# Optimization experiments

Hardware: AMD Instinct MI355X
Metric: run time of the kernel (lower is better)

## Reference

```python
import jax, jax.numpy as jnp
import numpy as np
import math

B, P, N, DM, H, DK, DH, DF = 2, 12, 170, 64, 8, 8, 32, 256
SQ = math.sqrt(DK)

def _ln(x, g, b):
    m = jnp.mean(x, -1, keepdims=True)
    v = jnp.var(x, -1, keepdims=True)
    return (x - m) / jnp.sqrt(v + 1e-5) * g + b

def _nozero_softmax(s):
    # faithful to nozero_softmax: mask = (s != 0), max over full row, +1e-5 in denom
    mask = (s != 0).astype(s.dtype)
    e = jnp.exp(s - jnp.max(s, -1, keepdims=True)) * mask
    return e / (jnp.sum(e, -1, keepdims=True) + 1e-5)

def _meta(c, w1, b1, w2, b2):
    # MetaLearner: [B,P,N,DM] -> [3,B,P,N,H,DK,DM]
    h = jax.nn.relu(c @ w1 + b1) @ w2 + b2
    h = h.reshape(c.shape[:3] + (3, H, DK, DM))
    return jnp.moveaxis(h, 3, 0)

def _mhlin(W, x):
    # multihead_linear_transform: per-position meta weight applied to x
    return jnp.einsum('bpnhkd,bpnd->bpnhk', W, x)

def _gdc(data, W1, W2):
    # Gated_Dynamic_Connection (noGC=False). data: [G,B,P,N,C]
    d = jnp.moveaxis(data, 0, 3)  # [B,P,N,G,C]
    a = jnp.einsum('bpngc,gcd->bpngd', d, W1)
    s = jax.nn.softmax(jax.nn.relu(jnp.einsum('bpngc,gcd->bpngd', d, W2)), axis=3)
    return jnp.sum(a * s, axis=3)  # [B,P,N,DM]

def _swish_gate(x, out, wg, bg, wo, bo):
    h = (x @ wg + bg) * out
    return (h * jax.nn.sigmoid(h)) @ wo + bo

def _spatial(Q, K, V, T):
    # adjacency-masked spatial attention. Dense-masked form is exactly the
    # scatter-into-zeros buffer of the original: zero where T==0, QK/sqrt(dk) on edges.
    s = jnp.einsum('bpihk,bpjhk->bphij', Q, K) / SQ
    Tb = T if T.ndim == 2 else T[:, :, None]  # adaptive graph [B,P,1,N,N]
    s = s * (Tb != 0)
    alpha = _nozero_softmax(s) * Tb
    return jnp.einsum('bphij,bpjhk->hbpik', alpha, V)  # [H,B,P,N,DK]

def _temporal(Q, K, V):
    s = jnp.einsum('bqnhk,bpnhk->bnhqp', Q, K) / SQ
    alpha = jax.nn.softmax(s, -1)
    return jnp.einsum('bnhqp,bpnhk->hbqnk', alpha, V)  # [H,B,P,N,DK]

def _retnet(Q, K, V, D):
    # multihead_temporal_regnet with g=1 leading dim folded in
    r = jnp.einsum('bqnhk,bpnhk->bnhqp', Q, K) / SQ
    r = r * D  # D: [H,P,P] causal decay
    rs = jnp.maximum(jnp.abs(jnp.sum(r, -1, keepdims=True)), 1.0)
    r = r / rs
    return jnp.einsum('bnhqp,bpnhk->hbqnk', r, V)  # [H,B,P,N,DK]

def _forward(x, c_x, enc, T, A, D, mr_w1, mr_b1, mr_w2, mr_b2, ms0_w1, ms0_b1, ms0_w2, ms0_b2, ms1_w1, ms1_b1, ms1_w2, ms1_b2, gr_W1, gr_W2, gs0_W1, gs0_W2, gs1_W1, gs1_W2, g2_W1, g2_W2, ge_W1, ge_W2, swr_wg, swr_bg, swr_wo, swr_bo, sws_wg, sws_bg, sws_wo, sws_bo, swe_wg, swe_bg, swe_wo, swe_bo, lnr_g, lnr_b, lns_g, lns_b, lne_g, lne_b, lnf_g, lnf_b, wq, wk, wv, f_w1, f_b1, f_w2, f_b2):
    # 1) RetNet-style temporal self retention (meta-learned QKV)
    W = _meta(c_x, mr_w1, mr_b1, mr_w2, mr_b2)
    o = _gdc(_retnet(_mhlin(W[0], x), _mhlin(W[1], x), _mhlin(W[2], x), D), gr_W1, gr_W2)
    o = _swish_gate(x, o, swr_wg, swr_bg, swr_wo, swr_bo)
    x1 = _ln(o + x, lnr_g, lnr_b)
    # 2) Spatial self attention: predefined graph + adaptive graph branches
    W0 = _meta(c_x, ms0_w1, ms0_b1, ms0_w2, ms0_b2)
    o0 = _gdc(_spatial(_mhlin(W0[0], x1), _mhlin(W0[1], x1), _mhlin(W0[2], x1), T), gs0_W1, gs0_W2)
    W1m = _meta(c_x, ms1_w1, ms1_b1, ms1_w2, ms1_b2)
    o1 = _gdc(_spatial(_mhlin(W1m[0], x1), _mhlin(W1m[1], x1), _mhlin(W1m[2], x1), A), gs1_W1, gs1_W2)
    o = _gdc(jnp.stack([o0, o1], 0), g2_W1, g2_W2)
    o = _swish_gate(x1, o, sws_wg, sws_bg, sws_wo, sws_bo)
    x2 = _ln(o + x1, lns_g, lns_b)
    # 3) Temporal encoder-decoder attention
    q = (x2 @ wq).reshape(B, P, N, H, DK)
    k = (enc @ wk).reshape(B, P, N, H, DK)
    v = (enc @ wv).reshape(B, P, N, H, DK)
    o = _gdc(_temporal(q, k, v), ge_W1, ge_W2)
    o = _swish_gate(x2, o, swe_wg, swe_bg, swe_wo, swe_bo)
    x3 = _ln(o + x2, lne_g, lne_b)
    # 4) FFN
    o = jax.nn.relu(x3 @ f_w1 + f_b1) @ f_w2 + f_b2
    return _ln(o + x3, lnf_g, lnf_b)


def setup_inputs() -> dict:
    key = jax.random.key(0)
    ks = iter(jax.random.split(key, 100))
    def rn(shape, s=0.05):
        return (jax.random.normal(next(ks), shape) * s).astype(jnp.float32)
    inp = {}
    inp['x'] = jax.random.normal(next(ks), (B, P, N, DM), jnp.float32)
    inp['c_x'] = jax.random.normal(next(ks), (B, P, N, DM), jnp.float32)
    inp['enc'] = jax.random.normal(next(ks), (B, P, N, DM), jnp.float32)
    mT = jax.random.uniform(next(ks), (N, N)) < 0.1
    inp['T'] = (jax.random.uniform(next(ks), (N, N)) * mT).astype(jnp.float32)
    mA = jax.random.uniform(next(ks), (B, P, N, N)) < 0.05
    inp['A'] = (jax.random.uniform(next(ks), (B, P, N, N)) * mA).astype(jnp.float32)
    q = np.arange(P)
    gam = 1.0 - 2.0 ** (-5.0 - np.arange(H))
    Dm = np.where(q[:, None] >= q[None, :], gam[:, None, None] ** (q[:, None] - q[None, :]), 0.0)
    inp['D'] = jnp.asarray(Dm, jnp.float32)  # [H,P,P]
    for p in ['mr', 'ms0', 'ms1']:
        inp[p + '_w1'] = rn((DM, DH)); inp[p + '_b1'] = jnp.zeros((DH,), jnp.float32)
        inp[p + '_w2'] = rn((DH, 3 * H * DK * DM)); inp[p + '_b2'] = jnp.zeros((3 * H * DK * DM,), jnp.float32)
    for p in ['gr', 'gs0', 'gs1', 'ge']:
        inp[p + '_W1'] = rn((H, DK, DM)); inp[p + '_W2'] = rn((H, DK, DM))
    inp['g2_W1'] = rn((2, DM, DM)); inp['g2_W2'] = rn((2, DM, DM))
    for p in ['swr', 'sws', 'swe']:
        inp[p + '_wg'] = rn((DM, DM)); inp[p + '_bg'] = jnp.zeros((DM,), jnp.float32)
        inp[p + '_wo'] = rn((DM, DM)); inp[p + '_bo'] = jnp.zeros((DM,), jnp.float32)
    for p in ['lnr', 'lns', 'lne', 'lnf']:
        inp[p + '_g'] = jnp.ones((DM,), jnp.float32); inp[p + '_b'] = jnp.zeros((DM,), jnp.float32)
    inp['wq'] = rn((DM, DM)); inp['wk'] = rn((DM, DM)); inp['wv'] = rn((DM, DM))
    inp['f_w1'] = rn((DM, DF)); inp['f_b1'] = jnp.zeros((DF,), jnp.float32)
    inp['f_w2'] = rn((DF, DM)); inp['f_b2'] = jnp.zeros((DM,), jnp.float32)
    return inp


def reference(x, c_x, enc, T, A, D, mr_w1, mr_b1, mr_w2, mr_b2, ms0_w1, ms0_b1, ms0_w2, ms0_b2, ms1_w1, ms1_b1, ms1_w2, ms1_b2, gr_W1, gr_W2, gs0_W1, gs0_W2, gs1_W1, gs1_W2, g2_W1, g2_W2, ge_W1, ge_W2, swr_wg, swr_bg, swr_wo, swr_bo, sws_wg, sws_bg, sws_wo, sws_bo, swe_wg, swe_bg, swe_wo, swe_bo, lnr_g, lnr_b, lns_g, lns_b, lne_g, lne_b, lnf_g, lnf_b, wq, wk, wv, f_w1, f_b1, f_w2, f_b2):
    return _forward(x, c_x, enc, T, A, D, mr_w1, mr_b1, mr_w2, mr_b2, ms0_w1, ms0_b1, ms0_w2, ms0_b2, ms1_w1, ms1_b1, ms1_w2, ms1_b2, gr_W1, gr_W2, gs0_W1, gs0_W2, gs1_W1, gs1_W2, g2_W1, g2_W2, ge_W1, ge_W2, swr_wg, swr_bg, swr_wo, swr_bo, sws_wg, sws_bg, sws_wo, sws_bo, swe_wg, swe_bg, swe_wo, swe_bo, lnr_g, lnr_b, lns_g, lns_b, lne_g, lne_b, lnf_g, lnf_b, wq, wk, wv, f_w1, f_b1, f_w2, f_b2)
```

## Files before the change

### kernel.cpp

```cpp
#include <hip/hip_runtime.h>
#include <hip/hip_bf16.h>
#include <math.h>

namespace {

constexpr int B_ = 2, P_ = 12, N_ = 170, DM_ = 64, H_ = 8, DK_ = 8, DH_ = 32, DF_ = 256;
constexpr int T_ = B_ * P_ * N_;
constexpr float SQRT_DK = 2.8284271247461903f;

constexpr int NG_ = 12;
constexpr int NC_ = 66;
constexpr int WFRAG_G = NG_ * NC_ * 64 * 8;

typedef __attribute__((ext_vector_type(4))) short short4v;
typedef __attribute__((ext_vector_type(8))) short short8v;
typedef __attribute__((ext_vector_type(4))) float float4v;

__device__ __forceinline__ unsigned short f2bf(float x) {
    union { float f; unsigned int u; } c; c.f = x;
    unsigned int r = (c.u + 0x7FFFu + ((c.u >> 16) & 1u)) >> 16;
    return (unsigned short)r;
}

__global__ void k_hr3(const float* __restrict__ c_x,
                      const float* __restrict__ w1a, const float* __restrict__ b1a,
                      const float* __restrict__ w1b, const float* __restrict__ b1b,
                      const float* __restrict__ w1c, const float* __restrict__ b1c,
                      float* __restrict__ hra, float* __restrict__ hrb,
                      float* __restrict__ hrc) {
    int z = blockIdx.y;
    const float* w1 = z == 0 ? w1a : (z == 1 ? w1b : w1c);
    const float* b1 = z == 0 ? b1a : (z == 1 ? b1b : b1c);
    float* hr = z == 0 ? hra : (z == 1 ? hrb : hrc);
    int idx = blockIdx.x * 256 + threadIdx.x;
    if (idx >= T_ * DH_) return;
    int t = idx / DH_, j = idx % DH_;
    float acc = b1[j];
    const float* cx = c_x + t * DM_;
    #pragma unroll
    for (int d = 0; d < DM_; ++d) acc += cx[d] * w1[d * DH_ + j];
    hr[idx] = fmaxf(acc, 0.f);
}

__global__ void k_wconv(const float* __restrict__ w2a, const float* __restrict__ b2a,
                        const float* __restrict__ w2b, const float* __restrict__ b2b,
                        const float* __restrict__ w2c, const float* __restrict__ b2c,
                        unsigned short* __restrict__ Wfrag) {
    int idx = blockIdx.x * 256 + threadIdx.x;
    if (idx >= 3 * NG_ * NC_ * 64) return;
    int lane = idx & 63;
    int c = (idx >> 6) % NC_;
    int ng = (idx >> 6) / NC_ % NG_;
    int g = idx / (64 * NC_ * NG_);
    const float* w2 = g == 0 ? w2a : (g == 1 ? w2b : w2c);
    const float* b2 = g == 0 ? b2a : (g == 1 ? b2b : b2c);
    int m = ng * 16 + (lane & 15);
    int u = c >> 1;
    int d0 = (c & 1) * 32 + (lane >> 4) * 8;
    const float* src = (u < DH_) ? (w2 + u * 12288 + m * 64 + d0) : (b2 + m * 64 + d0);
    short8v o;
    #pragma unroll
    for (int j = 0; j < 8; ++j) o[j] = (short)f2bf(src[j]);
    *(short8v*)(Wfrag + (size_t)idx * 8) = o;
}

__global__ __launch_bounds__(256) void k_meta_gemm2(
    const float* __restrict__ hr0, const float* __restrict__ hr1,
    const float* __restrict__ xin,
    const unsigned short* __restrict__ Wf0, const unsigned short* __restrict__ Wf1,
    float* __restrict__ out0, float* __restrict__ out1) {
    const int bz = blockIdx.z;
    const float* hr = bz ? hr1 : hr0;
    const unsigned short* Wf = bz ? Wf1 : Wf0;
    float* out = bz ? out1 : out0;

    const int tid = threadIdx.x;
    const int wv = tid >> 6, lane = tid & 63;
    const int l15 = lane & 15, quad = lane >> 4;
    const int g16 = blockIdx.x * 4 + wv;
    if (g16 >= 255) return;
    const int t = g16 * 16 + l15;
    const int nb = blockIdx.y;

    const float* xp = xin + t * 64 + quad * 8;
    float4v xa = *(const float4v*)(xp);
    float4v xb = *(const float4v*)(xp + 4);
    float4v xc = *(const float4v*)(xp + 32);
    float4v xd = *(const float4v*)(xp + 36);
    float xr[16] = {xa.x, xa.y, xa.z, xa.w, xb.x, xb.y, xb.z, xb.w,
                    xc.x, xc.y, xc.z, xc.w, xd.x, xd.y, xd.z, xd.w};

    const float* hrp = hr + t * 32;
    float4v acc[4] = {{0.f,0.f,0.f,0.f},{0.f,0.f,0.f,0.f},
                      {0.f,0.f,0.f,0.f},{0.f,0.f,0.f,0.f}};

    const unsigned short* wb = Wf + ((size_t)(nb * 4) * NC_ * 64 + lane) * 8;
    const size_t qstride = (size_t)NC_ * 64 * 8;
    const size_t cstride = 64 * 8;

    for (int u = 0; u < 33; ++u) {
        float hrv = (u < DH_) ? hrp[u] : 1.0f;
        short8v a0, a1;
        #pragma unroll
        for (int j = 0; j < 8; ++j) {
            a0[j] = (short)f2bf(hrv * xr[j]);
            a1[j] = (short)f2bf(hrv * xr[8 + j]);
        }
        const unsigned short* wc = wb + (size_t)(2 * u) * cstride;
        #pragma unroll
        for (int q = 0; q < 4; ++q) {
            short8v b0 = *(const short8v*)(wc + q * qstride);
            short8v b1 = *(const short8v*)(wc + q * qstride + cstride);
            acc[q] = __builtin_amdgcn_mfma_f32_16x16x32_bf16(a0, b0, acc[q], 0, 0, 0);
            acc[q] = __builtin_amdgcn_mfma_f32_16x16x32_bf16(a1, b1, acc[q], 0, 0, 0);
        }
    }

    #pragma unroll
    for (int q = 0; q < 4; ++q) {
        #pragma unroll
        for (int r = 0; r < 4; ++r) {
            int tt = g16 * 16 + quad * 4 + r;
            out[tt * 192 + nb * 64 + q * 16 + l15] = acc[q][r];
        }
    }
}

__global__ __launch_bounds__(256) void k_retnet(const float* __restrict__ qkv,
                                                const float* __restrict__ Dm,
                                                float* __restrict__ att) {
    const int bn = blockIdx.x;
    const int b = bn / N_, n = bn % N_;
    __shared__ float S[12][192];
    __shared__ float Ds[8 * 145];
    const int tid = threadIdx.x;
    for (int e = tid; e < 12 * 192; e += 256) {
        int p = e / 192, c = e % 192;
        S[p][c] = qkv[((size_t)((b * P_ + p) * N_ + n)) * 192 + c];
    }
    for (int e = tid; e < 1152; e += 256) {
        Ds[(e / 144) * 145 + (e % 144)] = Dm[e];
    }
    __syncthreads();
    const int qq = tid >> 6;
    const int lane = tid & 63;
    const int h = lane >> 3, k = lane & 7;
    for (int q = qq; q < P_; q += 4) {
        float Qv = S[q][h * 8 + k];
        float r[P_];
        float rsum = 0.f;
        #pragma unroll
        for (int p = 0; p < P_; ++p) {
            float prod = Qv * S[p][64 + h * 8 + k];
            prod += __shfl_xor(prod, 1, 64);
            prod += __shfl_xor(prod, 2, 64);
            prod += __shfl_xor(prod, 4, 64);
            float s = (prod / SQRT_DK) * Ds[h * 145 + q * 12 + p];
            r[p] = s; rsum += s;
        }
        float rs = fmaxf(fabsf(rsum), 1.0f);
        float acc = 0.f;
        #pragma unroll
        for (int p = 0; p < P_; ++p) acc += (r[p] / rs) * S[p][128 + h * 8 + k];
        att[((size_t)((b * P_ + q) * N_ + n)) * 64 + lane] = acc;
    }
}

__global__ __launch_bounds__(256) void k_temporal(const float* __restrict__ qkv,
                                                  float* __restrict__ att) {
    const int bn = blockIdx.x;
    const int b = bn / N_, n = bn % N_;
    __shared__ float S[12][192];
    const int tid = threadIdx.x;
    for (int e = tid; e < 12 * 192; e += 256) {
        int p = e / 192, c = e % 192;
        S[p][c] = qkv[((size_t)((b * P_ + p) * N_ + n)) * 192 + c];
    }
    __syncthreads();
    const int qq = tid >> 6;
    const int lane = tid & 63;
    const int h = lane >> 3, k = lane & 7;
    for (int q = qq; q < P_; q += 4) {
        float Qv = S[q][h * 8 + k];
        float s[P_];
        float mx = -1e30f;
        #pragma unroll
        for (int p = 0; p < P_; ++p) {
            float prod = Qv * S[p][64 + h * 8 + k];
            prod += __shfl_xor(prod, 1, 64);
            prod += __shfl_xor(prod, 2, 64);
            prod += __shfl_xor(prod, 4, 64);
            float v = prod / SQRT_DK;
            s[p] = v; mx = fmaxf(mx, v);
        }
        float den = 0.f, acc = 0.f;
        #pragma unroll
        for (int p = 0; p < P_; ++p) {
            float e = expf(s[p] - mx);
            den += e;
            acc += e * S[p][128 + h * 8 + k];
        }
        att[((size_t)((b * P_ + q) * N_ + n)) * 64 + lane] = acc / den;
    }
}

__global__ __launch_bounds__(256) void k_spatial4(
    const float* __restrict__ qkvA, const float* __restrict__ qkvB,
    const float* __restrict__ Tm, const float* __restrict__ Am,
    float* __restrict__ attA, float* __restrict__ attB) {
    const int bp = blockIdx.x;
    const int h = blockIdx.y;
    const int g = blockIdx.z >> 2;
    const int ic = blockIdx.z & 3;
    const float* qkv = g ? qkvB : qkvA;
    float* att = g ? attB : attA;

    __shared__ float sKt[8][192];
    __shared__ float sV[192][8];
    __shared__ float sW[4][192];

    const int tid = threadIdx.x;
    for (int e = tid; e < 384; e += 256) {
        int j = e >> 1, kh = (e & 1) * 4;
        float4v k4 = {0.f, 0.f, 0.f, 0.f}, v4 = k4;
        if (j < N_) {
            const float* row = qkv + (size_t)(bp * N_ + j) * 192 + h * 8 + kh;
            k4 = *(const float4v*)(row + 64);
            v4 = *(const float4v*)(row + 128);
        }
        sKt[kh + 0][j] = k4.x;
        sKt[kh + 1][j] = k4.y;
        sKt[kh + 2][j] = k4.z;
        sKt[kh + 3][j] = k4.w;
        *(float4v*)&sV[j][kh] = v4;
    }
    __syncthreads();

    const int wv = tid >> 6;
    const int lane = tid & 63;
    const int j8 = lane >> 3, kk = lane & 7;

    const int i0 = ic * 43;
    const int i1 = (i0 + 43 < N_) ? (i0 + 43) : N_;

    for (int i = i0 + wv; i < i1; i += 4) {
        const float* qrow = qkv + (size_t)(bp * N_ + i) * 192 + h * 8;
        float4v qa = *(const float4v*)qrow;
        float4v qb = *(const float4v*)(qrow + 4);
        float Qi[8] = {qa.x, qa.y, qa.z, qa.w, qb.x, qb.y, qb.z, qb.w};
        const float* Trow = g ? (Am + (size_t)(bp * N_ + i) * N_) : (Tm + (size_t)i * N_);

        float sloc[3], tloc[3];
        float mx = -1e30f;
        #pragma unroll
        for (int c = 0; c < 3; ++c) {
            int j = c * 64 + lane;
            float tv = 0.f, s = -1e30f;
            if (j < N_) {
                tv = Trow[j];
                if (tv != 0.f) {
                    float dot = 0.f;
                    #pragma unroll
                    for (int k = 0; k < 8; ++k) dot += Qi[k] * sKt[k][j];
                    s = dot / SQRT_DK;
                } else {
                    s = 0.f;
                }
            }
            sloc[c] = s; tloc[c] = tv;
            mx = fmaxf(mx, s);
        }
        #pragma unroll
        for (int off = 1; off < 64; off <<= 1) mx = fmaxf(mx, __shfl_xor(mx, off, 64));

        float den = 0.f;
        #pragma unroll
        for (int c = 0; c < 3; ++c) {
            float s = sloc[c];
            float e = (s != 0.f) ? expf(s - mx) : 0.f;
            den += e;
            sW[wv][c * 64 + lane] = e * tloc[c];
        }
        #pragma unroll
        for (int off = 1; off < 64; off <<= 1) den += __shfl_xor(den, off, 64);

        float acc = 0.f;
        #pragma unroll 4
        for (int j = j8; j < 192; j += 8) acc += sW[wv][j] * sV[j][kk];
        acc += __shfl_xor(acc, 8, 64);
        acc += __shfl_xor(acc, 16, 64);
        acc += __shfl_xor(acc, 32, 64);
        if (lane < 8)
            att[(size_t)(bp * N_ + i) * 64 + h * 8 + lane] = acc / (den + 1e-5f);
    }
}

__device__ __forceinline__ float gdc8(const float* dv, const float* W1,
                                      const float* W2, int dm) {
    float a[8], s[8];
    #pragma unroll
    for (int g = 0; g < 8; ++g) {
        float aa = 0.f, ss = 0.f;
        #pragma unroll
        for (int c = 0; c < 8; ++c) {
            float d = dv[g * 8 + c];
            aa += d * W1[(g * 8 + c) * 64 + dm];
            ss += d * W2[(g * 8 + c) * 64 + dm];
        }
        a[g] = aa; s[g] = fmaxf(ss, 0.f);
    }
    float mx = s[0];
    #pragma unroll
    for (int g = 1; g < 8; ++g) mx = fmaxf(mx, s[g]);
    float den = 0.f, o = 0.f;
    #pragma unroll
    for (int g = 0; g < 8; ++g) { float e = expf(s[g] - mx); den += e; o += a[g] * e; }
    return o / den;
}

__device__ __forceinline__ float ln_out(float r, int dm, const float* g, const float* b) {
    float m = r, m2 = r * r;
    #pragma unroll
    for (int off = 32; off; off >>= 1) { m += __shfl_xor(m, off, 64); m2 += __shfl_xor(m2, off, 64); }
    m *= (1.f / 64.f); m2 *= (1.f / 64.f);
    float var = m2 - m * m;
    return (r - m) * rsqrtf(var + 1e-5f) * g[dm] + b[dm];
}

__global__ __launch_bounds__(64) void k_gsl(const float* __restrict__ att, const float* __restrict__ xin,
    const float* W1, const float* W2,
    const float* wg, const float* bg,
    const float* wo, const float* bo,
    const float* lng, const float* lnb, float* __restrict__ xout) {
    int t = blockIdx.x, dm = threadIdx.x;
    __shared__ float dv[64], xv[64], swv[64];
    dv[dm] = att[t * 64 + dm];
    xv[dm] = xin[t * 64 + dm];
    __syncthreads();
    float o = gdc8(dv, W1, W2, dm);
    float hg = bg[dm];
    #pragma unroll
    for (int d = 0; d < 64; ++d) hg += xv[d] * wg[d * 64 + dm];
    hg *= o;
    swv[dm] = hg / (1.f + expf(-hg));
    __syncthreads();
    float ov = bo[dm];
    #pragma unroll
    for (int d = 0; d < 64; ++d) ov += swv[d] * wo[d * 64 + dm];
    float r = ov + xv[dm];
    xout[t * 64 + dm] = ln_out(r, dm, lng, lnb);
}

__global__ __launch_bounds__(64) void k_spatial_fuse(
    const float* __restrict__ att0, const float* __restrict__ att1, const float* __restrict__ x1,
    const float* gs0_W1, const float* gs0_W2,
    const float* gs1_W1, const float* gs1_W2,
    const float* g2_W1, const float* g2_W2,
    const float* wg, const float* bg,
    const float* wo, const float* bo,
    const float* lng, const float* lnb, float* __restrict__ xout) {
    int t = blockIdx.x, dm = threadIdx.x;
    __shared__ float d0[64], d1[64], o0s[64], o1s[64], xv[64], swv[64];
    d0[dm] = att0[t * 64 + dm];
    d1[dm] = att1[t * 64 + dm];
    xv[dm] = x1[t * 64 + dm];
    __syncthreads();
    o0s[dm] = gdc8(d0, gs0_W1, gs0_W2, dm);
    o1s[dm] = gdc8(d1, gs1_W1, gs1_W2, dm);
    __syncthreads();
    float a0 = 0.f, s0 = 0.f, a1 = 0.f, s1 = 0.f;
    #pragma unroll
    for (int c = 0; c < 64; ++c) {
        a0 += o0s[c] * g2_W1[c * 64 + dm];
        s0 += o0s[c] * g2_W2[c * 64 + dm];
        a1 += o1s[c] * g2_W1[(64 + c) * 64 + dm];
        s1 += o1s[c] * g2_W2[(64 + c) * 64 + dm];
    }
    s0 = fmaxf(s0, 0.f); s1 = fmaxf(s1, 0.f);
    float mx = fmaxf(s0, s1);
    float e0 = expf(s0 - mx), e1 = expf(s1 - mx);
    float o = (a0 * e0 + a1 * e1) / (e0 + e1);
    float hg = bg[dm];
    #pragma unroll
    for (int d = 0; d < 64; ++d) hg += xv[d] * wg[d * 64 + dm];
    hg *= o;
    swv[dm] = hg / (1.f + expf(-hg));
    __syncthreads();
    float ov = bo[dm];
    #pragma unroll
    for (int d = 0; d < 64; ++d) ov += swv[d] * wo[d * 64 + dm];
    float r = ov + xv[dm];
    xout[t * 64 + dm] = ln_out(r, dm, lng, lnb);
}

__global__ __launch_bounds__(64) void k_qkvproj(const float* __restrict__ x2,
    const float* __restrict__ enc,
    const float* wq, const float* wk, const float* wv,
    float* __restrict__ qkv) {
    int t = blockIdx.x, dm = threadIdx.x;
    __shared__ float xv[64], ev[64];
    xv[dm] = x2[t * 64 + dm];
    ev[dm] = enc[t * 64 + dm];
    __syncthreads();
    float aq = 0.f, ak = 0.f, av = 0.f;
    #pragma unroll
    for (int d = 0; d < 64; ++d) {
        aq += xv[d] * wq[d * 64 + dm];
        ak += ev[d] * wk[d * 64 + dm];
        av += ev[d] * wv[d * 64 + dm];
    }
    qkv[t * 192 + dm] = aq;
    qkv[t * 192 + 64 + dm] = ak;
    qkv[t * 192 + 128 + dm] = av;
}

__global__ __launch_bounds__(64) void k_ffn(const float* __restrict__ x3,
    const float* w1, const float* b1,
    const float* w2, const float* b2,
    const float* lng, const float* lnb,
    float* __restrict__ out) {
    int t = blockIdx.x, dm = threadIdx.x;
    __shared__ float xv[64], hv[256];
    xv[dm] = x3[t * 64 + dm];
    __syncthreads();
    #pragma unroll
    for (int e = 0; e < 4; ++e) {
        int j = e * 64 + dm;
        float a = b1[j];
        #pragma unroll
        for (int d = 0; d < 64; ++d) a += xv[d] * w1[d * 256 + j];
        hv[j] = fmaxf(a, 0.f);
    }
    __syncthreads();
    float a = b2[dm];
    for (int j = 0; j < 256; ++j) a += hv[j] * w2[j * 64 + dm];
    float r = a + xv[dm];
    out[t * 64 + dm] = ln_out(r, dm, lng, lnb);
}

}

extern "C" void kernel_launch(void* const* d_in, const int* in_sizes, int n_in,
                              void* d_out, int out_size, void* d_ws, size_t ws_size,
                              hipStream_t stream) {
    (void)in_sizes; (void)n_in; (void)out_size; (void)ws_size;
    const float* x    = (const float*)d_in[0];
    const float* c_x  = (const float*)d_in[1];
    const float* enc  = (const float*)d_in[2];
    const float* Tm   = (const float*)d_in[3];
    const float* Am   = (const float*)d_in[4];
    const float* Dm   = (const float*)d_in[5];
    const float* mr_w1 = (const float*)d_in[6];
    const float* mr_b1 = (const float*)d_in[7];
    const float* mr_w2 = (const float*)d_in[8];
    const float* mr_b2 = (const float*)d_in[9];
    const float* ms0_w1 = (const float*)d_in[10];
    const float* ms0_b1 = (const float*)d_in[11];
    const float* ms0_w2 = (const float*)d_in[12];
    const float* ms0_b2 = (const float*)d_in[13];
    const float* ms1_w1 = (const float*)d_in[14];
    const float* ms1_b1 = (const float*)d_in[15];
    const float* ms1_w2 = (const float*)d_in[16];
    const float* ms1_b2 = (const float*)d_in[17];
    const float* gr_W1 = (const float*)d_in[18];
    const float* gr_W2 = (const float*)d_in[19];
    const float* gs0_W1 = (const float*)d_in[20];
    const float* gs0_W2 = (const float*)d_in[21];
    const float* gs1_W1 = (const float*)d_in[22];
    const float* gs1_W2 = (const float*)d_in[23];
    const float* g2_W1 = (const float*)d_in[24];
    const float* g2_W2 = (const float*)d_in[25];
    const float* ge_W1 = (const float*)d_in[26];
    const float* ge_W2 = (const float*)d_in[27];
    const float* swr_wg = (const float*)d_in[28];
    const float* swr_bg = (const float*)d_in[29];
    const float* swr_wo = (const float*)d_in[30];
    const float* swr_bo = (const float*)d_in[31];
    const float* sws_wg = (const float*)d_in[32];
    const float* sws_bg = (const float*)d_in[33];
    const float* sws_wo = (const float*)d_in[34];
    const float* sws_bo = (const float*)d_in[35];
    const float* swe_wg = (const float*)d_in[36];
    const float* swe_bg = (const float*)d_in[37];
    const float* swe_wo = (const float*)d_in[38];
    const float* swe_bo = (const float*)d_in[39];
    const float* lnr_g = (const float*)d_in[40];
    const float* lnr_b = (const float*)d_in[41];
    const float* lns_g = (const float*)d_in[42];
    const float* lns_b = (const float*)d_in[43];
    const float* lne_g = (const float*)d_in[44];
    const float* lne_b = (const float*)d_in[45];
    const float* lnf_g = (const float*)d_in[46];
    const float* lnf_b = (const float*)d_in[47];
    const float* wq = (const float*)d_in[48];
    const float* wk = (const float*)d_in[49];
    const float* wv = (const float*)d_in[50];
    const float* f_w1 = (const float*)d_in[51];
    const float* f_b1 = (const float*)d_in[52];
    const float* f_w2 = (const float*)d_in[53];
    const float* f_b2 = (const float*)d_in[54];

    float* ws   = (float*)d_ws;
    float* hr   = ws;
    float* hr2  = hr   + T_ * DH_;
    float* qkva = hr2  + T_ * DH_;
    float* qkvb = qkva + T_ * 192;
    float* atta = qkvb + T_ * 192;
    float* attb = atta + T_ * DM_;
    float* x1f  = attb + T_ * DM_;
    float* x2f  = x1f  + T_ * DM_;
    float* x3f  = x2f  + T_ * DM_;
    unsigned short* Wfrag = (unsigned short*)(x3f + T_ * DM_);
    float* hr_r = attb;

    k_wconv<<<(3 * NG_ * NC_ * 64 + 255) / 256, 256, 0, stream>>>(
        mr_w2, mr_b2, ms0_w2, ms0_b2, ms1_w2, ms1_b2, Wfrag);

    k_hr3<<<dim3(510, 3), 256, 0, stream>>>(c_x, mr_w1, mr_b1, ms0_w1, ms0_b1,
                                            ms1_w1, ms1_b1, hr_r, hr, hr2);

    k_meta_gemm2<<<dim3(64, 3, 1), 256, 0, stream>>>(
        hr_r, hr_r, x, Wfrag, Wfrag, qkva, qkva);
    k_retnet<<<B_ * N_, 256, 0, stream>>>(qkva, Dm, atta);
    k_gsl<<<T_, 64, 0, stream>>>(atta, x, gr_W1, gr_W2, swr_wg, swr_bg, swr_wo, swr_bo,
                                 lnr_g, lnr_b, x1f);

    k_meta_gemm2<<<dim3(64, 3, 2), 256, 0, stream>>>(
        hr, hr2, x1f, Wfrag + WFRAG_G, Wfrag + 2 * WFRAG_G, qkva, qkvb);
    k_spatial4<<<dim3(B_ * P_, H_, 8), 256, 0, stream>>>(qkva, qkvb, Tm, Am, atta, attb);
    k_spatial_fuse<<<T_, 64, 0, stream>>>(atta, attb, x1f, gs0_W1, gs0_W2, gs1_W1, gs1_W2,
                                          g2_W1, g2_W2, sws_wg, sws_bg, sws_wo, sws_bo,
                                          lns_g, lns_b, x2f);

    k_qkvproj<<<T_, 64, 0, stream>>>(x2f, enc, wq, wk, wv, qkva);
    k_temporal<<<B_ * N_, 256, 0, stream>>>(qkva, atta);
    k_gsl<<<T_, 64, 0, stream>>>(atta, x2f, ge_W1, ge_W2, swe_wg, swe_bg, swe_wo, swe_bo,
                                 lne_g, lne_b, x3f);

    k_ffn<<<T_, 64, 0, stream>>>(x3f, f_w1, f_b1, f_w2, f_b2, lnf_g, lnf_b, (float*)d_out);
}
```

Measured before the change: 344.7 us.

## Port token-wise dense layers to bf16 MFMA with pre-packed weight fragments

Replaces the five per-token scalar kernels (gated dynamic connection, swish-gate, spatial fuse, QKV projection, FFN with layer norm) with MFMA 16x16x32 bf16 kernels that process 16 tokens per wave. A new conversion kernel packs all small weight matrices into bf16 fragment layout, with block-diagonal padding for the grouped GDC weights, so they feed MFMA directly. The aim is to cut scalar FMA work and the 4080 tiny-block launches. In exchange, activations and weights are rounded to bf16, which lowers precision. The GDC softmax also drops max-subtraction, relying on small logits.

After: 345.0 us. Within noise of the previous version (+0.1%).

```diff
diff --git a/kernel.cpp b/kernel.cpp
--- a/kernel.cpp
+++ b/kernel.cpp
@@ -11,6 +11,8 @@
 constexpr int NG_ = 12;
 constexpr int NC_ = 66;
 constexpr int WFRAG_G = NG_ * NC_ * 64 * 8;
+
+constexpr int WSM_UNITS = 53;
 
 typedef __attribute__((ext_vector_type(4))) short short4v;
 typedef __attribute__((ext_vector_type(8))) short short8v;
@@ -20,6 +22,18 @@
     union { float f; unsigned int u; } c; c.f = x;
     unsigned int r = (c.u + 0x7FFFu + ((c.u >> 16) & 1u)) >> 16;
     return (unsigned short)r;
+}
+
+__device__ __forceinline__ short8v afrag(const float* rowbase, int kc, int quad) {
+    const float* p = rowbase + kc * 32 + quad * 8;
+    float4v a = *(const float4v*)p;
+    float4v b = *(const float4v*)(p + 4);
+    short8v f;
+    f[0] = (short)f2bf(a.x); f[1] = (short)f2bf(a.y);
+    f[2] = (short)f2bf(a.z); f[3] = (short)f2bf(a.w);
+    f[4] = (short)f2bf(b.x); f[5] = (short)f2bf(b.y);
+    f[6] = (short)f2bf(b.z); f[7] = (short)f2bf(b.w);
+    return f;
 }
 
 __global__ void k_hr3(const float* __restrict__ c_x,
@@ -64,6 +78,69 @@
     *(short8v*)(Wfrag + (size_t)idx * 8) = o;
 }
 
+__global__ void k_wconv2(
+    const float* swr_wg, const float* swr_wo, const float* sws_wg, const float* sws_wo,
+    const float* swe_wg, const float* swe_wo,
+    const float* wq, const float* wk, const float* wv,
+    const float* f_w1, const float* f_w2,
+    const float* g2_W1, const float* g2_W2,
+    const float* gr_W1, const float* gr_W2, const float* gs0_W1, const float* gs0_W2,
+    const float* gs1_W1, const float* gs1_W2, const float* ge_W1, const float* ge_W2,
+    unsigned short* __restrict__ Wsm) {
+    const int job = blockIdx.y;
+    const int idx = blockIdx.x * 256 + threadIdx.x;
+    const float* s1 = nullptr; const float* s2 = nullptr;
+    int dst = 0, KC = 2, NG = 4, N = 64, kind = 0;
+    switch (job) {
+        case 0:  s1 = swr_wg; dst = 0; break;
+        case 1:  s1 = swr_wo; dst = 1; break;
+        case 2:  s1 = sws_wg; dst = 2; break;
+        case 3:  s1 = sws_wo; dst = 3; break;
+        case 4:  s1 = swe_wg; dst = 4; break;
+        case 5:  s1 = swe_wo; dst = 5; break;
+        case 6:  s1 = wq; dst = 6; break;
+        case 7:  s1 = wk; dst = 7; break;
+        case 8:  s1 = wv; dst = 8; break;
+        case 9:  s1 = f_w1; dst = 9;  NG = 16; N = 256; break;
+        case 10: s1 = f_w2; dst = 13; KC = 8; break;
+        case 11: s1 = g2_W1;        dst = 17; break;
+        case 12: s1 = g2_W1 + 4096; dst = 18; break;
+        case 13: s1 = g2_W2;        dst = 19; break;
+        case 14: s1 = g2_W2 + 4096; dst = 20; break;
+        case 15: s1 = gr_W1;  s2 = gr_W2;  dst = 21; kind = 1; break;
+        case 16: s1 = gs0_W1; s2 = gs0_W2; dst = 29; kind = 1; break;
+        case 17: s1 = gs1_W1; s2 = gs1_W2; dst = 37; kind = 1; break;
+        default: s1 = ge_W1;  s2 = ge_W2;  dst = 45; kind = 1; break;
+    }
+    if (kind == 0) {
+        if (idx >= NG * KC * 64) return;
+        int lane = idx & 63;
+        int kc = (idx >> 6) % KC, ng = (idx >> 6) / KC;
+        int krow = kc * 32 + (lane >> 4) * 8;
+        int n = ng * 16 + (lane & 15);
+        short8v o;
+        #pragma unroll
+        for (int j = 0; j < 8; ++j) o[j] = (short)f2bf(s1[(krow + j) * N + n]);
+        *(short8v*)(Wsm + (size_t)dst * 4096 + (size_t)idx * 8) = o;
+    } else {
+        if (idx >= 8 * 4 * 64) return;
+        int lane = idx & 63;
+        int ng = (idx >> 6) & 3, g = idx >> 8;
+        int quad = lane >> 4, n = ng * 16 + (lane & 15);
+        short8v o1 = {0,0,0,0,0,0,0,0}, o2 = {0,0,0,0,0,0,0,0};
+        if (quad == (g & 3)) {
+            #pragma unroll
+            for (int j = 0; j < 8; ++j) {
+                o1[j] = (short)f2bf(s1[(g * 8 + j) * 64 + n]);
+                o2[j] = (short)f2bf(s2[(g * 8 + j) * 64 + n]);
+            }
+        }
+        size_t off = (size_t)dst * 4096 + (size_t)idx * 8;
+        *(short8v*)(Wsm + off) = o1;
+        *(short8v*)(Wsm + off + 16384) = o2;
+    }
+}
+
 __global__ __launch_bounds__(256) void k_meta_gemm2(
     const float* __restrict__ hr0, const float* __restrict__ hr1,
     const float* __restrict__ xin,
@@ -295,147 +372,387 @@
     }
 }
 
-__device__ __forceinline__ float gdc8(const float* dv, const float* W1,
-                                      const float* W2, int dm) {
-    float a[8], s[8];
-    #pragma unroll
+__device__ __forceinline__ void gdc_mfma(const short8v* attf,
+                                         const unsigned short* gdcW, int lane,
+                                         float4v* num, float4v* den) {
+    #pragma unroll
+    for (int q = 0; q < 4; ++q) {
+        num[q] = (float4v){0.f, 0.f, 0.f, 0.f};
+        den[q] = (float4v){0.f, 0.f, 0.f, 0.f};
+    }
     for (int g = 0; g < 8; ++g) {
-        float aa = 0.f, ss = 0.f;
-        #pragma unroll
-        for (int c = 0; c < 8; ++c) {
-            float d = dv[g * 8 + c];
-            aa += d * W1[(g * 8 + c) * 64 + dm];
-            ss += d * W2[(g * 8 + c) * 64 + dm];
-        }
-        a[g] = aa; s[g] = fmaxf(ss, 0.f);
-    }
-    float mx = s[0];
-    #pragma unroll
-    for (int g = 1; g < 8; ++g) mx = fmaxf(mx, s[g]);
-    float den = 0.f, o = 0.f;
-    #pragma unroll
-    for (int g = 0; g < 8; ++g) { float e = expf(s[g] - mx); den += e; o += a[g] * e; }
-    return o / den;
-}
-
-__device__ __forceinline__ float ln_out(float r, int dm, const float* g, const float* b) {
-    float m = r, m2 = r * r;
-    #pragma unroll
-    for (int off = 32; off; off >>= 1) { m += __shfl_xor(m, off, 64); m2 += __shfl_xor(m2, off, 64); }
-    m *= (1.f / 64.f); m2 *= (1.f / 64.f);
-    float var = m2 - m * m;
-    return (r - m) * rsqrtf(var + 1e-5f) * g[dm] + b[dm];
-}
-
-__global__ __launch_bounds__(64) void k_gsl(const float* __restrict__ att, const float* __restrict__ xin,
-    const float* W1, const float* W2,
-    const float* wg, const float* bg,
-    const float* wo, const float* bo,
-    const float* lng, const float* lnb, float* __restrict__ xout) {
-    int t = blockIdx.x, dm = threadIdx.x;
-    __shared__ float dv[64], xv[64], swv[64];
-    dv[dm] = att[t * 64 + dm];
-    xv[dm] = xin[t * 64 + dm];
-    __syncthreads();
-    float o = gdc8(dv, W1, W2, dm);
-    float hg = bg[dm];
-    #pragma unroll
-    for (int d = 0; d < 64; ++d) hg += xv[d] * wg[d * 64 + dm];
-    hg *= o;
-    swv[dm] = hg / (1.f + expf(-hg));
-    __syncthreads();
-    float ov = bo[dm];
-    #pragma unroll
-    for (int d = 0; d < 64; ++d) ov += swv[d] * wo[d * 64 + dm];
-    float r = ov + xv[dm];
-    xout[t * 64 + dm] = ln_out(r, dm, lng, lnb);
-}
-
-__global__ __launch_bounds__(64) void k_spatial_fuse(
-    const float* __restrict__ att0, const float* __restrict__ att1, const float* __restrict__ x1,
-    const float* gs0_W1, const float* gs0_W2,
-    const float* gs1_W1, const float* gs1_W2,
-    const float* g2_W1, const float* g2_W2,
-    const float* wg, const float* bg,
-    const float* wo, const float* bo,
-    const float* lng, const float* lnb, float* __restrict__ xout) {
-    int t = blockIdx.x, dm = threadIdx.x;
-    __shared__ float d0[64], d1[64], o0s[64], o1s[64], xv[64], swv[64];
-    d0[dm] = att0[t * 64 + dm];
-    d1[dm] = att1[t * 64 + dm];
-    xv[dm] = x1[t * 64 + dm];
-    __syncthreads();
-    o0s[dm] = gdc8(d0, gs0_W1, gs0_W2, dm);
-    o1s[dm] = gdc8(d1, gs1_W1, gs1_W2, dm);
-    __syncthreads();
-    float a0 = 0.f, s0 = 0.f, a1 = 0.f, s1 = 0.f;
-    #pragma unroll
-    for (int c = 0; c < 64; ++c) {
-        a0 += o0s[c] * g2_W1[c * 64 + dm];
-        s0 += o0s[c] * g2_W2[c * 64 + dm];
-        a1 += o1s[c] * g2_W1[(64 + c) * 64 + dm];
-        s1 += o1s[c] * g2_W2[(64 + c) * 64 + dm];
-    }
-    s0 = fmaxf(s0, 0.f); s1 = fmaxf(s1, 0.f);
-    float mx = fmaxf(s0, s1);
-    float e0 = expf(s0 - mx), e1 = expf(s1 - mx);
-    float o = (a0 * e0 + a1 * e1) / (e0 + e1);
-    float hg = bg[dm];
-    #pragma unroll
-    for (int d = 0; d < 64; ++d) hg += xv[d] * wg[d * 64 + dm];
-    hg *= o;
-    swv[dm] = hg / (1.f + expf(-hg));
-    __syncthreads();
-    float ov = bo[dm];
-    #pragma unroll
-    for (int d = 0; d < 64; ++d) ov += swv[d] * wo[d * 64 + dm];
-    float r = ov + xv[dm];
-    xout[t * 64 + dm] = ln_out(r, dm, lng, lnb);
-}
-
-__global__ __launch_bounds__(64) void k_qkvproj(const float* __restrict__ x2,
-    const float* __restrict__ enc,
-    const float* wq, const float* wk, const float* wv,
+        const unsigned short* wb = gdcW + ((size_t)(g * 4) * 64 + lane) * 8;
+        short8v af = attf[g >> 2];
+        float4v a[4], s[4];
+        #pragma unroll
+        for (int q = 0; q < 4; ++q) {
+            a[q] = (float4v){0.f, 0.f, 0.f, 0.f};
+            s[q] = (float4v){0.f, 0.f, 0.f, 0.f};
+        }
+        #pragma unroll
+        for (int q = 0; q < 4; ++q) {
+            short8v b1 = *(const short8v*)(wb + q * 512);
+            short8v b2 = *(const short8v*)(wb + 16384 + q * 512);
+            a[q] = __builtin_amdgcn_mfma_f32_16x16x32_bf16(af, b1, a[q], 0, 0, 0);
+            s[q] = __builtin_amdgcn_mfma_f32_16x16x32_bf16(af, b2, s[q], 0, 0, 0);
+        }
+        #pragma unroll
+        for (int q = 0; q < 4; ++q) {
+            #pragma unroll
+            for (int r = 0; r < 4; ++r) {
+                float e = __expf(fmaxf(s[q][r], 0.f));
+                den[q][r] += e;
+                num[q][r] += a[q][r] * e;
+            }
+        }
+    }
+}
+
+__global__ __launch_bounds__(256) void k_gsl5(
+    const float* __restrict__ att, const float* __restrict__ xin,
+    const unsigned short* __restrict__ gdcW,
+    const unsigned short* __restrict__ gateW, const unsigned short* __restrict__ woW,
+    const float* __restrict__ bg, const float* __restrict__ bo,
+    const float* __restrict__ lng, const float* __restrict__ lnb,
+    float* __restrict__ xout) {
+    __shared__ unsigned short swl[4][16][72];
+    const int tid = threadIdx.x, wv = tid >> 6, lane = tid & 63;
+    const int l15 = lane & 15, quad = lane >> 4;
+    const int g16 = blockIdx.x * 4 + wv;
+    if (g16 >= 255) return;
+    const int t = g16 * 16 + l15;
+
+    short8v attf[2], xf[2];
+    #pragma unroll
+    for (int kc = 0; kc < 2; ++kc) {
+        attf[kc] = afrag(att + (size_t)t * 64, kc, quad);
+        xf[kc]   = afrag(xin + (size_t)t * 64, kc, quad);
+    }
+
+    float4v num[4], den[4];
+    gdc_mfma(attf, gdcW, lane, num, den);
+
+    float4v hg[4];
+    #pragma unroll
+    for (int q = 0; q < 4; ++q) hg[q] = (float4v){0.f, 0.f, 0.f, 0.f};
+    #pragma unroll
+    for (int kc = 0; kc < 2; ++kc)
+        #pragma unroll
+        for (int q = 0; q < 4; ++q)
+            hg[q] = __builtin_amdgcn_mfma_f32_16x16x32_bf16(
+                xf[kc], *(const short8v*)(gateW + ((size_t)(q * 2 + kc) * 64 + lane) * 8),
+                hg[q], 0, 0, 0);
+
+    float bgq[4];
+    #pragma unroll
+    for (int q = 0; q < 4; ++q) bgq[q] = bg[q * 16 + l15];
+    #pragma unroll
+    for (int q = 0; q < 4; ++q)
+        #pragma unroll
+        for (int r = 0; r < 4; ++r) {
+            float v = (hg[q][r] + bgq[q]) * (num[q][r] / den[q][r]);
+            float sw = v / (1.f + __expf(-v));
+            swl[wv][quad * 4 + r][q * 16 + l15] = f2bf(sw);
+        }
+    short8v swf0 = *(const short8v*)&swl[wv][l15][quad * 8];
+    short8v swf1 = *(const short8v*)&swl[wv][l15][32 + quad * 8];
+
+    float4v ov[4];
+    #pragma unroll
+    for (int q = 0; q < 4; ++q) ov[q] = (float4v){0.f, 0.f, 0.f, 0.f};
+    #pragma unroll
+    for (int q = 0; q < 4; ++q) {
+        ov[q] = __builtin_amdgcn_mfma_f32_16x16x32_bf16(
+            swf0, *(const short8v*)(woW + ((size_t)(q * 2 + 0) * 64 + lane) * 8), ov[q], 0, 0, 0);
+        ov[q] = __builtin_amdgcn_mfma_f32_16x16x32_bf16(
+            swf1, *(const short8v*)(woW + ((size_t)(q * 2 + 1) * 64 + lane) * 8), ov[q], 0, 0, 0);
+    }
+
+    float boq[4], lgq[4], lbq[4];
+    #pragma unroll
+    for (int q = 0; q < 4; ++q) {
+        boq[q] = bo[q * 16 + l15]; lgq[q] = lng[q * 16 + l15]; lbq[q] = lnb[q * 16 + l15];
+    }
+    float v[4][4];
+    #pragma unroll
+    for (int q = 0; q < 4; ++q)
+        #pragma unroll
+        for (int r = 0; r < 4; ++r)
+            v[q][r] = ov[q][r] + boq[q]
+                    + xin[(size_t)(g16 * 16 + quad * 4 + r) * 64 + q * 16 + l15];
+    #pragma unroll
+    for (int r = 0; r < 4; ++r) {
+        float s1 = 0.f, s2 = 0.f;
+        #pragma unroll
+        for (int q = 0; q < 4; ++q) { s1 += v[q][r]; s2 += v[q][r] * v[q][r]; }
+        #pragma unroll
+        for (int off = 1; off < 16; off <<= 1) {
+            s1 += __shfl_xor(s1, off, 64);
+            s2 += __shfl_xor(s2, off, 64);
+        }
+        float m = s1 * (1.f / 64.f);
+        float var = s2 * (1.f / 64.f) - m * m;
+        float inv = rsqrtf(var + 1e-5f);
+        int tt = g16 * 16 + quad * 4 + r;
+        #pragma unroll
+        for (int q = 0; q < 4; ++q)
+            xout[(size_t)tt * 64 + q * 16 + l15] = (v[q][r] - m) * inv * lgq[q] + lbq[q];
+    }
+}
+
+__global__ __launch_bounds__(256) void k_spatial_fuse5(
+    const float* __restrict__ att0, const float* __restrict__ att1,
+    const float* __restrict__ x1,
+    const unsigned short* __restrict__ gdc0W, const unsigned short* __restrict__ gdc1W,
+    const unsigned short* __restrict__ g2W1a, const unsigned short* __restrict__ g2W1b,
+    const unsigned short* __restrict__ g2W2a, const unsigned short* __restrict__ g2W2b,
+    const unsigned short* __restrict__ gateW, const unsigned short* __restrict__ woW,
+    const float* __restrict__ bg, const float* __restrict__ bo,
+    const float* __restrict__ lng, const float* __restrict__ lnb,
+    float* __restrict__ xout) {
+    __shared__ unsigned short o0l[4][16][72], o1l[4][16][72], swl[4][16][72];
+    const int tid = threadIdx.x, wv = tid >> 6, lane = tid & 63;
+    const int l15 = lane & 15, quad = lane >> 4;
+    const int g16 = blockIdx.x * 4 + wv;
+    if (g16 >= 255) return;
+    const int t = g16 * 16 + l15;
+
+    short8v a0f[2], a1f[2], xf[2];
+    #pragma unroll
+    for (int kc = 0; kc < 2; ++kc) {
+        a0f[kc] = afrag(att0 + (size_t)t * 64, kc, quad);
+        a1f[kc] = afrag(att1 + (size_t)t * 64, kc, quad);
+        xf[kc]  = afrag(x1   + (size_t)t * 64, kc, quad);
+    }
+    {
+        float4v n0[4], d0[4];
+        gdc_mfma(a0f, gdc0W, lane, n0, d0);
+        #pragma unroll
+        for (int q = 0; q < 4; ++q)
+            #pragma unroll
+            for (int r = 0; r < 4; ++r)
+                o0l[wv][quad * 4 + r][q * 16 + l15] = f2bf(n0[q][r] / d0[q][r]);
+    }
+    {
+        float4v n1[4], d1[4];
+        gdc_mfma(a1f, gdc1W, lane, n1, d1);
+        #pragma unroll
+        for (int q = 0; q < 4; ++q)
+            #pragma unroll
+            for (int r = 0; r < 4; ++r)
+                o1l[wv][quad * 4 + r][q * 16 + l15] = f2bf(n1[q][r] / d1[q][r]);
+    }
+    short8v o0f[2], o1f[2];
+    o0f[0] = *(const short8v*)&o0l[wv][l15][quad * 8];
+    o0f[1] = *(const short8v*)&o0l[wv][l15][32 + quad * 8];
+    o1f[0] = *(const short8v*)&o1l[wv][l15][quad * 8];
+    o1f[1] = *(const short8v*)&o1l[wv][l15][32 + quad * 8];
+
+    float4v A0[4], S0[4], A1[4], S1[4];
+    #pragma unroll
+    for (int q = 0; q < 4; ++q) {
+        A0[q] = (float4v){0.f,0.f,0.f,0.f}; S0[q] = A0[q]; A1[q] = A0[q]; S1[q] = A0[q];
+    }
+    #pragma unroll
+    for (int kc = 0; kc < 2; ++kc)
+        #pragma unroll
+        for (int q = 0; q < 4; ++q) {
+            size_t fo = ((size_t)(q * 2 + kc) * 64 + lane) * 8;
+            A0[q] = __builtin_amdgcn_mfma_f32_16x16x32_bf16(o0f[kc], *(const short8v*)(g2W1a + fo), A0[q], 0, 0, 0);
+            S0[q] = __builtin_amdgcn_mfma_f32_16x16x32_bf16(o0f[kc], *(const short8v*)(g2W2a + fo), S0[q], 0, 0, 0);
+            A1[q] = __builtin_amdgcn_mfma_f32_16x16x32_bf16(o1f[kc], *(const short8v*)(g2W1b + fo), A1[q], 0, 0, 0);
+            S1[q] = __builtin_amdgcn_mfma_f32_16x16x32_bf16(o1f[kc], *(const short8v*)(g2W2b + fo), S1[q], 0, 0, 0);
+        }
+    float og[4][4];
+    #pragma unroll
+    for (int q = 0; q < 4; ++q)
+        #pragma unroll
+        for (int r = 0; r < 4; ++r) {
+            float e0 = __expf(fmaxf(S0[q][r], 0.f));
+            float e1 = __expf(fmaxf(S1[q][r], 0.f));
+            og[q][r] = (A0[q][r] * e0 + A1[q][r] * e1) / (e0 + e1);
+        }
+
+    float4v hg[4];
+    #pragma unroll
+    for (int q = 0; q < 4; ++q) hg[q] = (float4v){0.f,0.f,0.f,0.f};
+    #pragma unroll
+    for (int kc = 0; kc < 2; ++kc)
+        #pragma unroll
+        for (int q = 0; q < 4; ++q)
+            hg[q] = __builtin_amdgcn_mfma_f32_16x16x32_bf16(
+                xf[kc], *(const short8v*)(gateW + ((size_t)(q * 2 + kc) * 64 + lane) * 8),
+                hg[q], 0, 0, 0);
+    float bgq[4];
+    #pragma unroll
+    for (int q = 0; q < 4; ++q) bgq[q] = bg[q * 16 + l15];
+    #pragma unroll
+    for (int q = 0; q < 4; ++q)
+        #pragma unroll
+        for (int r = 0; r < 4; ++r) {
+            float vv = (hg[q][r] + bgq[q]) * og[q][r];
+            float sw = vv / (1.f + __expf(-vv));
+            swl[wv][quad * 4 + r][q * 16 + l15] = f2bf(sw);
+        }
+    short8v swf0 = *(const short8v*)&swl[wv][l15][quad * 8];
+    short8v swf1 = *(const short8v*)&swl[wv][l15][32 + quad * 8];
+
+    float4v ov[4];
+    #pragma unroll
+    for (int q = 0; q < 4; ++q) ov[q] = (float4v){0.f,0.f,0.f,0.f};
+    #pragma unroll
+    for (int q = 0; q < 4; ++q) {
+        ov[q] = __builtin_amdgcn_mfma_f32_16x16x32_bf16(
+            swf0, *(const short8v*)(woW + ((size_t)(q * 2 + 0) * 64 + lane) * 8), ov[q], 0, 0, 0);
+        ov[q] = __builtin_amdgcn_mfma_f32_16x16x32_bf16(
+            swf1, *(const short8v*)(woW + ((size_t)(q * 2 + 1) * 64 + lane) * 8), ov[q], 0, 0, 0);
+    }
+    float boq[4], lgq[4], lbq[4];
+    #pragma unroll
+    for (int q = 0; q < 4; ++q) {
+        boq[q] = bo[q * 16 + l15]; lgq[q] = lng[q * 16 + l15]; lbq[q] = lnb[q * 16 + l15];
+    }
+    float v[4][4];
+    #pragma unroll
+    for (int q = 0; q < 4; ++q)
+        #pragma unroll
+        for (int r = 0; r < 4; ++r)
+            v[q][r] = ov[q][r] + boq[q]
+                    + x1[(size_t)(g16 * 16 + quad * 4 + r) * 64 + q * 16 + l15];
+    #pragma unroll
+    for (int r = 0; r < 4; ++r) {
+        float s1 = 0.f, s2 = 0.f;
+        #pragma unroll
+        for (int q = 0; q < 4; ++q) { s1 += v[q][r]; s2 += v[q][r] * v[q][r]; }
+        #pragma unroll
+        for (int off = 1; off < 16; off <<= 1) {
+            s1 += __shfl_xor(s1, off, 64);
+            s2 += __shfl_xor(s2, off, 64);
+        }
+        float m = s1 * (1.f / 64.f);
+        float var = s2 * (1.f / 64.f) - m * m;
+        float inv = rsqrtf(var + 1e-5f);
+        int tt = g16 * 16 + quad * 4 + r;
+        #pragma unroll
+        for (int q = 0; q < 4; ++q)
+            xout[(size_t)tt * 64 + q * 16 + l15] = (v[q][r] - m) * inv * lgq[q] + lbq[q];
+    }
+}
+
+__global__ __launch_bounds__(256) void k_qkvproj5(
+    const float* __restrict__ x2, const float* __restrict__ enc,
+    const unsigned short* __restrict__ wqF, const unsigned short* __restrict__ wkF,
+    const unsigned short* __restrict__ wvF,
     float* __restrict__ qkv) {
-    int t = blockIdx.x, dm = threadIdx.x;
-    __shared__ float xv[64], ev[64];
-    xv[dm] = x2[t * 64 + dm];
-    ev[dm] = enc[t * 64 + dm];
-    __syncthreads();
-    float aq = 0.f, ak = 0.f, av = 0.f;
-    #pragma unroll
-    for (int d = 0; d < 64; ++d) {
-        aq += xv[d] * wq[d * 64 + dm];
-        ak += ev[d] * wk[d * 64 + dm];
-        av += ev[d] * wv[d * 64 + dm];
-    }
-    qkv[t * 192 + dm] = aq;
-    qkv[t * 192 + 64 + dm] = ak;
-    qkv[t * 192 + 128 + dm] = av;
-}
-
-__global__ __launch_bounds__(64) void k_ffn(const float* __restrict__ x3,
-    const float* w1, const float* b1,
-    const float* w2, const float* b2,
-    const float* lng, const float* lnb,
+    const int tid = threadIdx.x, wv = tid >> 6, lane = tid & 63;
+    const int l15 = lane & 15, quad = lane >> 4;
+    const int g16 = blockIdx.x * 4 + wv;
+    if (g16 >= 255) return;
+    const int t = g16 * 16 + l15;
+    short8v xf[2], ef[2];
+    #pragma unroll
+    for (int kc = 0; kc < 2; ++kc) {
+        xf[kc] = afrag(x2 + (size_t)t * 64, kc, quad);
+        ef[kc] = afrag(enc + (size_t)t * 64, kc, quad);
+    }
+    #pragma unroll
+    for (int seg = 0; seg < 3; ++seg) {
+        const unsigned short* W = seg == 0 ? wqF : (seg == 1 ? wkF : wvF);
+        const short8v* af = seg == 0 ? xf : ef;
+        float4v ac[4];
+        #pragma unroll
+        for (int q = 0; q < 4; ++q) ac[q] = (float4v){0.f,0.f,0.f,0.f};
+        #pragma unroll
+        for (int kc = 0; kc < 2; ++kc)
+            #pragma unroll
+            for (int q = 0; q < 4; ++q)
+                ac[q] = __builtin_amdgcn_mfma_f32_16x16x32_bf16(
+                    af[kc], *(const short8v*)(W + ((size_t)(q * 2 + kc) * 64 + lane) * 8),
+                    ac[q], 0, 0, 0);
+        #pragma unroll
+        for (int q = 0; q < 4; ++q)
+            #pragma unroll
+            for (int r = 0; r < 4; ++r)
+                qkv[(size_t)(g16 * 16 + quad * 4 + r) * 192 + seg * 64 + q * 16 + l15]
+                    = ac[q][r];
+    }
+}
+
+__global__ __launch_bounds__(256) void k_ffn5(
+    const float* __restrict__ x3,
+    const unsigned short* __restrict__ w1F, const float* __restrict__ b1,
+    const unsigned short* __restrict__ w2F, const float* __restrict__ b2,
+    const float* __restrict__ lng, const float* __restrict__ lnb,
     float* __restrict__ out) {
-    int t = blockIdx.x, dm = threadIdx.x;
-    __shared__ float xv[64], hv[256];
-    xv[dm] = x3[t * 64 + dm];
-    __syncthreads();
-    #pragma unroll
-    for (int e = 0; e < 4; ++e) {
-        int j = e * 64 + dm;
-        float a = b1[j];
-        #pragma unroll
-        for (int d = 0; d < 64; ++d) a += xv[d] * w1[d * 256 + j];
-        hv[j] = fmaxf(a, 0.f);
-    }
-    __syncthreads();
-    float a = b2[dm];
-    for (int j = 0; j < 256; ++j) a += hv[j] * w2[j * 64 + dm];
-    float r = a + xv[dm];
-    out[t * 64 + dm] = ln_out(r, dm, lng, lnb);
+    __shared__ unsigned short hl[4][16][264];
+    const int tid = threadIdx.x, wv = tid >> 6, lane = tid & 63;
+    const int l15 = lane & 15, quad = lane >> 4;
+    const int g16 = blockIdx.x * 4 + wv;
+    if (g16 >= 255) return;
+    const int t = g16 * 16 + l15;
+    short8v xf[2];
+    xf[0] = afrag(x3 + (size_t)t * 64, 0, quad);
+    xf[1] = afrag(x3 + (size_t)t * 64, 1, quad);
+
+    float4v h[16];
+    #pragma unroll
+    for (int ng = 0; ng < 16; ++ng) h[ng] = (float4v){0.f,0.f,0.f,0.f};
+    #pragma unroll
+    for (int kc = 0; kc < 2; ++kc)
+        #pragma unroll
+        for (int ng = 0; ng < 16; ++ng)
+            h[ng] = __builtin_amdgcn_mfma_f32_16x16x32_bf16(
+                xf[kc], *(const short8v*)(w1F + ((size_t)(ng * 2 + kc) * 64 + lane) * 8),
+                h[ng], 0, 0, 0);
+    #pragma unroll
+    for (int ng = 0; ng < 16; ++ng) {
+        float b1v = b1[ng * 16 + l15];
+        #pragma unroll
+        for (int r = 0; r < 4; ++r)
+            hl[wv][quad * 4 + r][ng * 16 + l15] = f2bf(fmaxf(h[ng][r] + b1v, 0.f));
+    }
+    float4v ov[4];
+    #pragma unroll
+    for (int q = 0; q < 4; ++q) ov[q] = (float4v){0.f,0.f,0.f,0.f};
+    #pragma unroll
+    for (int kc = 0; kc < 8; ++kc) {
+        short8v hf = *(const short8v*)&hl[wv][l15][kc * 32 + quad * 8];
+        #pragma unroll
+        for (int q = 0; q < 4; ++q)
+            ov[q] = __builtin_amdgcn_mfma_f32_16x16x32_bf16(
+                hf, *(const short8v*)(w2F + ((size_t)(q * 8 + kc) * 64 + lane) * 8),
+                ov[q], 0, 0, 0);
+    }
+    float boq[4], lgq[4], lbq[4];
+    #pragma unroll
+    for (int q = 0; q < 4; ++q) {
+        boq[q] = b2[q * 16 + l15]; lgq[q] = lng[q * 16 + l15]; lbq[q] = lnb[q * 16 + l15];
+    }
+    float v[4][4];
+    #pragma unroll
+    for (int q = 0; q < 4; ++q)
+        #pragma unroll
+        for (int r = 0; r < 4; ++r)
+            v[q][r] = ov[q][r] + boq[q]
+                    + x3[(size_t)(g16 * 16 + quad * 4 + r) * 64 + q * 16 + l15];
+    #pragma unroll
+    for (int r = 0; r < 4; ++r) {
+        float s1 = 0.f, s2 = 0.f;
+        #pragma unroll
+        for (int q = 0; q < 4; ++q) { s1 += v[q][r]; s2 += v[q][r] * v[q][r]; }
+        #pragma unroll
+        for (int off = 1; off < 16; off <<= 1) {
+            s1 += __shfl_xor(s1, off, 64);
+            s2 += __shfl_xor(s2, off, 64);
+        }
+        float m = s1 * (1.f / 64.f);
+        float var = s2 * (1.f / 64.f) - m * m;
+        float inv = rsqrtf(var + 1e-5f);
+        int tt = g16 * 16 + quad * 4 + r;
+        #pragma unroll
+        for (int q = 0; q < 4; ++q)
+            out[(size_t)tt * 64 + q * 16 + l15] = (v[q][r] - m) * inv * lgq[q] + lbq[q];
+    }
 }
 
 }
@@ -511,10 +828,17 @@
     float* x2f  = x1f  + T_ * DM_;
     float* x3f  = x2f  + T_ * DM_;
     unsigned short* Wfrag = (unsigned short*)(x3f + T_ * DM_);
+    unsigned short* Wsm   = Wfrag + 3 * WFRAG_G;
     float* hr_r = attb;
+
+    auto U = [&](int i) { return (const unsigned short*)(Wsm + (size_t)i * 4096); };
 
     k_wconv<<<(3 * NG_ * NC_ * 64 + 255) / 256, 256, 0, stream>>>(
         mr_w2, mr_b2, ms0_w2, ms0_b2, ms1_w2, ms1_b2, Wfrag);
+    k_wconv2<<<dim3(8, 19), 256, 0, stream>>>(
+        swr_wg, swr_wo, sws_wg, sws_wo, swe_wg, swe_wo, wq, wk, wv, f_w1, f_w2,
+        g2_W1, g2_W2, gr_W1, gr_W2, gs0_W1, gs0_W2, gs1_W1, gs1_W2, ge_W1, ge_W2,
+        Wsm);
 
     k_hr3<<<dim3(510, 3), 256, 0, stream>>>(c_x, mr_w1, mr_b1, ms0_w1, ms0_b1,
                                             ms1_w1, ms1_b1, hr_r, hr, hr2);
@@ -522,20 +846,21 @@
     k_meta_gemm2<<<dim3(64, 3, 1), 256, 0, stream>>>(
         hr_r, hr_r, x, Wfrag, Wfrag, qkva, qkva);
     k_retnet<<<B_ * N_, 256, 0, stream>>>(qkva, Dm, atta);
-    k_gsl<<<T_, 64, 0, stream>>>(atta, x, gr_W1, gr_W2, swr_wg, swr_bg, swr_wo, swr_bo,
-                                 lnr_g, lnr_b, x1f);
+    k_gsl5<<<64, 256, 0, stream>>>(atta, x, U(21), U(0), U(1),
+                                   swr_bg, swr_bo, lnr_g, lnr_b, x1f);
 
     k_meta_gemm2<<<dim3(64, 3, 2), 256, 0, stream>>>(
         hr, hr2, x1f, Wfrag + WFRAG_G, Wfrag + 2 * WFRAG_G, qkva, qkvb);
     k_spatial4<<<dim3(B_ * P_, H_, 8), 256, 0, stream>>>(qkva, qkvb, Tm, Am, atta, attb);
-    k_spatial_fuse<<<T_, 64, 0, stream>>>(atta, attb, x1f, gs0_W1, gs0_W2, gs1_W1, gs1_W2,
-                                          g2_W1, g2_W2, sws_wg, sws_bg, sws_wo, sws_bo,
-                                          lns_g, lns_b, x2f);
-
-    k_qkvproj<<<T_, 64, 0, stream>>>(x2f, enc, wq, wk, wv, qkva);
+    k_spatial_fuse5<<<64, 256, 0, stream>>>(atta, attb, x1f,
+                                            U(29), U(37), U(17), U(18), U(19), U(20),
+                                            U(2), U(3), sws_bg, sws_bo, lns_g, lns_b, x2f);
+
+    k_qkvproj5<<<64, 256, 0, stream>>>(x2f, enc, U(6), U(7), U(8), qkva);
     k_temporal<<<B_ * N_, 256, 0, stream>>>(qkva, atta);
-    k_gsl<<<T_, 64, 0, stream>>>(atta, x2f, ge_W1, ge_W2, swe_wg, swe_bg, swe_wo, swe_bo,
-                                 lne_g, lne_b, x3f);
-
-    k_ffn<<<T_, 64, 0, stream>>>(x3f, f_w1, f_b1, f_w2, f_b2, lnf_g, lnf_b, (float*)d_out);
-}
+    k_gsl5<<<64, 256, 0, stream>>>(atta, x2f, U(45), U(4), U(5),
+                                   swe_bg, swe_bo, lne_g, lne_b, x3f);
+
+    k_ffn5<<<64, 256, 0, stream>>>(x3f, U(9), f_b1, U(13), f_b2, lnf_g, lnf_b,
+                                   (float*)d_out);
+}
```
